# Performance work log

Hardware: AMD Instinct MI355X
Metric: run time of the kernel (lower is better)

The kernel has to match this reference:

```python
import jax, jax.numpy as jnp
import numpy as np

B, T, H = 4096, 1024, 15


def setup_inputs() -> dict:
    key = jax.random.key(0)
    ks = jax.random.split(key, 7)
    return {
        "x": jax.random.normal(ks[0], (B, T, 1), dtype=jnp.float32),
        "w_ih": jax.random.normal(ks[1], (H, 1), dtype=jnp.float32) * (1.0 / np.sqrt(H)),
        "w_hh": jax.random.normal(ks[2], (H, H), dtype=jnp.float32) * (1.0 / np.sqrt(H)),
        "b_ih": jax.random.normal(ks[3], (H,), dtype=jnp.float32) * (1.0 / np.sqrt(H)),
        "b_hh": jax.random.normal(ks[4], (H,), dtype=jnp.float32) * (1.0 / np.sqrt(H)),
        "w_lin": jax.random.normal(ks[5], (1, H), dtype=jnp.float32) * (1.0 / np.sqrt(H)),
        "b_lin": jax.random.normal(ks[6], (1,), dtype=jnp.float32) * (1.0 / np.sqrt(H)),
    }


def reference(x, w_ih, w_hh, b_ih, b_hh, w_lin, b_lin):
    # Single-layer tanh RNN (batch_first), then per-timestep linear head.
    # Precompute the input projection for all timesteps: [B, T, H]
    xp = jnp.einsum("bti,hi->bth", x, w_ih) + b_ih + b_hh
    xp_t = jnp.swapaxes(xp, 0, 1)  # [T, B, H] for scan over time

    def step(h, xt):
        # h: [B, H], xt: [B, H]
        h_new = jnp.tanh(xt + h @ w_hh.T)
        return h_new, h_new

    h0 = jnp.zeros((x.shape[0], w_hh.shape[0]), dtype=x.dtype)
    _, hs = jax.lax.scan(step, h0, xp_t)  # hs: [T, B, H]
    hs = jnp.swapaxes(hs, 0, 1)  # [B, T, H]
    return jnp.einsum("bth,oh->bto", hs, w_lin) + b_lin  # [B, T, 1]
```

## Files before the change

kernel.cpp:

```cpp
#include <hip/hip_runtime.h>

#define B_ 4096
#define T_ 1024
#define H_ 15

#define STEP(XT, ODST)                                                        \
  do {                                                                        \
    float bs_, cB_, cC_, cD_, e_;                                             \
    asm("v_fma_f32 %[bs], %[xt], %[wih], %[bias]\n\t"                         \
        "v_mul_f32_dpp %[acc], %[u], %[w1] row_ror:1 row_mask:0xf bank_mask:0xf\n\t"  \
        "v_mul_f32_dpp %[cB], %[u], %[w2] row_ror:2 row_mask:0xf bank_mask:0xf\n\t"   \
        "v_mul_f32_dpp %[cC], %[u], %[w3] row_ror:3 row_mask:0xf bank_mask:0xf\n\t"   \
        "v_fma_f32 %[cD], %[u], %[w0], %[bs]\n\t"                             \
        "v_fmac_f32_dpp %[acc], %[u], %[w5] row_ror:5 row_mask:0xf bank_mask:0xf\n\t" \
        "v_fmac_f32_dpp %[cB], %[u], %[w6] row_ror:6 row_mask:0xf bank_mask:0xf\n\t"  \
        "v_fmac_f32_dpp %[cC], %[u], %[w7] row_ror:7 row_mask:0xf bank_mask:0xf\n\t"  \
        "v_fmac_f32_dpp %[cD], %[u], %[w4] row_ror:4 row_mask:0xf bank_mask:0xf\n\t"  \
        "v_fmac_f32_dpp %[acc], %[u], %[w9] row_ror:9 row_mask:0xf bank_mask:0xf\n\t" \
        "v_fmac_f32_dpp %[cB], %[u], %[w10] row_ror:10 row_mask:0xf bank_mask:0xf\n\t" \
        "v_fmac_f32_dpp %[cC], %[u], %[w11] row_ror:11 row_mask:0xf bank_mask:0xf\n\t" \
        "v_fmac_f32_dpp %[cD], %[u], %[w8] row_ror:8 row_mask:0xf bank_mask:0xf\n\t"  \
        "v_fmac_f32_dpp %[acc], %[u], %[w13] row_ror:13 row_mask:0xf bank_mask:0xf\n\t" \
        "v_fmac_f32_dpp %[cB], %[u], %[w14] row_ror:14 row_mask:0xf bank_mask:0xf\n\t" \
        "v_fmac_f32_dpp %[cC], %[u], %[w15] row_ror:15 row_mask:0xf bank_mask:0xf\n\t" \
        "v_fmac_f32_dpp %[cD], %[u], %[w12] row_ror:12 row_mask:0xf bank_mask:0xf\n\t" \
        "v_add_f32 %[acc], %[acc], %[cB]\n\t"                                 \
        "v_add_f32 %[cC], %[cC], %[cD]\n\t"                                   \
        "v_add_f32 %[acc], %[acc], %[cC]\n\t"                                 \
        "v_exp_f32 %[e], %[acc]\n\t"                                          \
        "s_nop 0\n\t"                                                         \
        "v_add_f32 %[e], 1.0, %[e]\n\t"                                       \
        "v_rcp_f32 %[u], %[e]\n\t"                                            \
        "s_nop 0\n\t"                                                         \
        : [u] "+v"(u), [acc] "=&v"(ODST), [bs] "=&v"(bs_), [cB] "=&v"(cB_),   \
          [cC] "=&v"(cC_), [cD] "=&v"(cD_), [e] "=&v"(e_)                     \
        : [xt] "v"(XT), [wih] "v"(wih2), [bias] "v"(bias2),                   \
          [w0] "v"(wr[0]), [w1] "v"(wr[1]), [w2] "v"(wr[2]),                  \
          [w3] "v"(wr[3]), [w4] "v"(wr[4]), [w5] "v"(wr[5]),                  \
          [w6] "v"(wr[6]), [w7] "v"(wr[7]), [w8] "v"(wr[8]),                  \
          [w9] "v"(wr[9]), [w10] "v"(wr[10]), [w11] "v"(wr[11]),              \
          [w12] "v"(wr[12]), [w13] "v"(wr[13]), [w14] "v"(wr[14]),            \
          [w15] "v"(wr[15]));                                                 \
  } while (0)

#define POS(K, XV)                                                            \
  do {                                                                        \
    float o_;                                                                 \
    STEP(XV, o_);                                                             \
    osta[((K) + 3) & 3] = o_;                                                 \
    if (((K) & 3) == 0) {                                                     \
      if ((K) > 0 || t > 0) {                                                 \
        if (m == 15)                                                          \
          *(float4*)(ob + t + (K) - 4) =                                      \
              make_float4(osta[0], osta[1], osta[2], osta[3]);                \
      }                                                                       \
    }                                                                         \
    if (((K) & 3) == 3) {                                                     \
      int _tn = t + 32 + (((K) >> 2) << 2);                                   \
      if (_tn >= T_) _tn = 0;          \
      qq[(K) >> 2] = *(const float4*)(xb + _tn);                              \
    }                                                                         \
  } while (0)

__global__ __attribute__((amdgpu_flat_work_group_size(256, 256),
                          amdgpu_waves_per_eu(1, 1)))
void rnn_tanh_kernel(
    const float* __restrict__ x, const float* __restrict__ w_ih,
    const float* __restrict__ w_hh, const float* __restrict__ b_ih,
    const float* __restrict__ b_hh, const float* __restrict__ w_lin,
    const float* __restrict__ b_lin, float* __restrict__ out) {
  const int tid = threadIdx.x;
  const int m = tid & 15;
  const int b = blockIdx.x * 16 + (tid >> 4);

  const float S = 2.8853900817779268f;

  float wsum = b_lin[0];
  for (int j = 0; j < H_; ++j) wsum += w_lin[j];
  const float C = wsum;

  float wr[16];
#pragma unroll
  for (int n = 0; n < 16; ++n) {
    const int c = (m - n) & 15;
    if (m < H_)
      wr[n] = (c < H_) ? -2.0f * S * w_hh[m * H_ + c] : 0.0f;
    else
      wr[n] = (c < H_) ? -2.0f * w_lin[c] : 0.0f;
  }
  float rowsum = 0.0f;
  if (m < H_)
    for (int j = 0; j < H_; ++j) rowsum += w_hh[m * H_ + j];
  const float wih2  = (m < H_) ? S * w_ih[m] : 0.0f;
  const float bias2 = (m < H_) ? S * (b_ih[m] + b_hh[m] + rowsum) : C;

  const float* xb = x + (size_t)b * T_;
  float* ob = out + (size_t)b * T_;

  float u = 0.5f;
  asm("s_nop 1" : "+v"(u));
  float osta[4];

  float4 qq[8];
#pragma unroll
  for (int j = 0; j < 8; ++j) qq[j] = *(const float4*)(xb + 4 * j);

  for (int t = 0; t < T_; t += 32) {
    POS(0,  qq[0].x); POS(1,  qq[0].y); POS(2,  qq[0].z); POS(3,  qq[0].w);
    POS(4,  qq[1].x); POS(5,  qq[1].y); POS(6,  qq[1].z); POS(7,  qq[1].w);
    POS(8,  qq[2].x); POS(9,  qq[2].y); POS(10, qq[2].z); POS(11, qq[2].w);
    POS(12, qq[3].x); POS(13, qq[3].y); POS(14, qq[3].z); POS(15, qq[3].w);
    POS(16, qq[4].x); POS(17, qq[4].y); POS(18, qq[4].z); POS(19, qq[4].w);
    POS(20, qq[5].x); POS(21, qq[5].y); POS(22, qq[5].z); POS(23, qq[5].w);
    POS(24, qq[6].x); POS(25, qq[6].y); POS(26, qq[6].z); POS(27, qq[6].w);
    POS(28, qq[7].x); POS(29, qq[7].y); POS(30, qq[7].z); POS(31, qq[7].w);
  }

  {
    float o_;
    STEP(0.0f, o_);
    osta[3] = o_;
    if (m == 15)
      *(float4*)(ob + T_ - 4) = make_float4(osta[0], osta[1], osta[2], osta[3]);
  }
}

extern "C" void kernel_launch(void* const* d_in, const int* in_sizes, int n_in,
                              void* d_out, int out_size, void* d_ws, size_t ws_size,
                              hipStream_t stream) {
  (void)in_sizes; (void)n_in; (void)out_size; (void)d_ws; (void)ws_size;
  rnn_tanh_kernel<<<B_ / 16, 256, 0, stream>>>(
      (const float*)d_in[0], (const float*)d_in[1], (const float*)d_in[2],
      (const float*)d_in[3], (const float*)d_in[4], (const float*)d_in[5],
      (const float*)d_in[6], (float*)d_out);
}
```

Before: 141.7 us.

## Split each RNN row's dot product across two lane halves with permlane16 swap

Each batch row now uses 32 lanes instead of 16. Each 16-lane half computes 8 of the 16 rotated recurrent products, and the two partial sums are combined with v_permlane16_swap plus a DPP row_ror:8 move. This halves the serial FMA chain per timestep and doubles the grid, with waves_per_eu raised to 2. The cost is extra cross-lane latency from the swap, the nops and the DPP move, and twice as many lanes per batch row.

After: 167.4 us. 1.18x slower.

```diff
diff --git a/kernel.cpp b/kernel.cpp
--- a/kernel.cpp
+++ b/kernel.cpp
@@ -6,41 +6,36 @@
 
 #define STEP(XT, ODST)                                                        \
   do {                                                                        \
-    float bs_, cB_, cC_, cD_, e_;                                             \
+    float bs_, cA_, cB_, cC_, cD_, e_;                                        \
     asm("v_fma_f32 %[bs], %[xt], %[wih], %[bias]\n\t"                         \
-        "v_mul_f32_dpp %[acc], %[u], %[w1] row_ror:1 row_mask:0xf bank_mask:0xf\n\t"  \
-        "v_mul_f32_dpp %[cB], %[u], %[w2] row_ror:2 row_mask:0xf bank_mask:0xf\n\t"   \
-        "v_mul_f32_dpp %[cC], %[u], %[w3] row_ror:3 row_mask:0xf bank_mask:0xf\n\t"   \
-        "v_fma_f32 %[cD], %[u], %[w0], %[bs]\n\t"                             \
-        "v_fmac_f32_dpp %[acc], %[u], %[w5] row_ror:5 row_mask:0xf bank_mask:0xf\n\t" \
-        "v_fmac_f32_dpp %[cB], %[u], %[w6] row_ror:6 row_mask:0xf bank_mask:0xf\n\t"  \
-        "v_fmac_f32_dpp %[cC], %[u], %[w7] row_ror:7 row_mask:0xf bank_mask:0xf\n\t"  \
-        "v_fmac_f32_dpp %[cD], %[u], %[w4] row_ror:4 row_mask:0xf bank_mask:0xf\n\t"  \
-        "v_fmac_f32_dpp %[acc], %[u], %[w9] row_ror:9 row_mask:0xf bank_mask:0xf\n\t" \
-        "v_fmac_f32_dpp %[cB], %[u], %[w10] row_ror:10 row_mask:0xf bank_mask:0xf\n\t" \
-        "v_fmac_f32_dpp %[cC], %[u], %[w11] row_ror:11 row_mask:0xf bank_mask:0xf\n\t" \
-        "v_fmac_f32_dpp %[cD], %[u], %[w8] row_ror:8 row_mask:0xf bank_mask:0xf\n\t"  \
-        "v_fmac_f32_dpp %[acc], %[u], %[w13] row_ror:13 row_mask:0xf bank_mask:0xf\n\t" \
-        "v_fmac_f32_dpp %[cB], %[u], %[w14] row_ror:14 row_mask:0xf bank_mask:0xf\n\t" \
-        "v_fmac_f32_dpp %[cC], %[u], %[w15] row_ror:15 row_mask:0xf bank_mask:0xf\n\t" \
-        "v_fmac_f32_dpp %[cD], %[u], %[w12] row_ror:12 row_mask:0xf bank_mask:0xf\n\t" \
-        "v_add_f32 %[acc], %[acc], %[cB]\n\t"                                 \
+        "v_fma_f32 %[cA], %[u], %[w0], %[bs]\n\t"                             \
+        "v_mul_f32_dpp %[cB], %[u], %[w1] row_ror:1 row_mask:0xf bank_mask:0xf\n\t" \
+        "v_mul_f32_dpp %[cC], %[u], %[w2] row_ror:2 row_mask:0xf bank_mask:0xf\n\t" \
+        "v_mul_f32_dpp %[cD], %[u], %[w3] row_ror:3 row_mask:0xf bank_mask:0xf\n\t" \
+        "v_fmac_f32_dpp %[cA], %[u], %[w4] row_ror:4 row_mask:0xf bank_mask:0xf\n\t" \
+        "v_fmac_f32_dpp %[cB], %[u], %[w5] row_ror:5 row_mask:0xf bank_mask:0xf\n\t" \
+        "v_fmac_f32_dpp %[cC], %[u], %[w6] row_ror:6 row_mask:0xf bank_mask:0xf\n\t" \
+        "v_fmac_f32_dpp %[cD], %[u], %[w7] row_ror:7 row_mask:0xf bank_mask:0xf\n\t" \
+        "v_add_f32 %[cA], %[cA], %[cB]\n\t"                                   \
         "v_add_f32 %[cC], %[cC], %[cD]\n\t"                                   \
-        "v_add_f32 %[acc], %[acc], %[cC]\n\t"                                 \
-        "v_exp_f32 %[e], %[acc]\n\t"                                          \
+        "v_add_f32 %[cA], %[cA], %[cC]\n\t"                                   \
+        "v_mov_b32 %[cB], %[cA]\n\t"                                          \
+        "s_nop 1\n\t"                                                         \
+        "v_permlane16_swap_b32 %[cB], %[cA]\n\t"                              \
+        "v_add_f32 %[a], %[cB], %[cA]\n\t"                                    \
+        "s_nop 1\n\t"                                                         \
+        "v_mov_b32_dpp %[a], %[a] row_ror:8 row_mask:0xa bank_mask:0xf\n\t"   \
+        "v_exp_f32 %[e], %[a]\n\t"                                            \
         "s_nop 0\n\t"                                                         \
         "v_add_f32 %[e], 1.0, %[e]\n\t"                                       \
         "v_rcp_f32 %[u], %[e]\n\t"                                            \
         "s_nop 0\n\t"                                                         \
-        : [u] "+v"(u), [acc] "=&v"(ODST), [bs] "=&v"(bs_), [cB] "=&v"(cB_),   \
-          [cC] "=&v"(cC_), [cD] "=&v"(cD_), [e] "=&v"(e_)                     \
+        : [u] "+v"(u), [a] "=&v"(ODST), [bs] "=&v"(bs_), [cA] "=&v"(cA_),     \
+          [cB] "=&v"(cB_), [cC] "=&v"(cC_), [cD] "=&v"(cD_), [e] "=&v"(e_)    \
         : [xt] "v"(XT), [wih] "v"(wih2), [bias] "v"(bias2),                   \
           [w0] "v"(wr[0]), [w1] "v"(wr[1]), [w2] "v"(wr[2]),                  \
           [w3] "v"(wr[3]), [w4] "v"(wr[4]), [w5] "v"(wr[5]),                  \
-          [w6] "v"(wr[6]), [w7] "v"(wr[7]), [w8] "v"(wr[8]),                  \
-          [w9] "v"(wr[9]), [w10] "v"(wr[10]), [w11] "v"(wr[11]),              \
-          [w12] "v"(wr[12]), [w13] "v"(wr[13]), [w14] "v"(wr[14]),            \
-          [w15] "v"(wr[15]));                                                 \
+          [w6] "v"(wr[6]), [w7] "v"(wr[7]));                                  \
   } while (0)
 
 #define POS(K, XV)                                                            \
@@ -50,7 +45,7 @@
     osta[((K) + 3) & 3] = o_;                                                 \
     if (((K) & 3) == 0) {                                                     \
       if ((K) > 0 || t > 0) {                                                 \
-        if (m == 15)                                                          \
+        if (mm == 15)                                                         \
           *(float4*)(ob + t + (K) - 4) =                                      \
               make_float4(osta[0], osta[1], osta[2], osta[3]);                \
       }                                                                       \
@@ -63,7 +58,7 @@
   } while (0)
 
 __global__ __attribute__((amdgpu_flat_work_group_size(256, 256),
-                          amdgpu_waves_per_eu(1, 1)))
+                          amdgpu_waves_per_eu(2, 2)))
 void rnn_tanh_kernel(
     const float* __restrict__ x, const float* __restrict__ w_ih,
     const float* __restrict__ w_hh, const float* __restrict__ b_ih,
@@ -71,7 +66,9 @@
     const float* __restrict__ b_lin, float* __restrict__ out) {
   const int tid = threadIdx.x;
   const int m = tid & 15;
-  const int b = blockIdx.x * 16 + (tid >> 4);
+  const int h = (tid >> 4) & 1;
+  const int mm = tid & 31;
+  const int b = blockIdx.x * 8 + (tid >> 5);
 
   const float S = 2.8853900817779268f;
 
@@ -79,10 +76,10 @@
   for (int j = 0; j < H_; ++j) wsum += w_lin[j];
   const float C = wsum;
 
-  float wr[16];
+  float wr[8];
 #pragma unroll
-  for (int n = 0; n < 16; ++n) {
-    const int c = (m - n) & 15;
+  for (int n = 0; n < 8; ++n) {
+    const int c = (m + 8 * h - n) & 15;
     if (m < H_)
       wr[n] = (c < H_) ? -2.0f * S * w_hh[m * H_ + c] : 0.0f;
     else
@@ -91,8 +88,9 @@
   float rowsum = 0.0f;
   if (m < H_)
     for (int j = 0; j < H_; ++j) rowsum += w_hh[m * H_ + j];
-  const float wih2  = (m < H_) ? S * w_ih[m] : 0.0f;
-  const float bias2 = (m < H_) ? S * (b_ih[m] + b_hh[m] + rowsum) : C;
+  const float wih2  = (h == 0 && m < H_) ? S * w_ih[m] : 0.0f;
+  const float bias2 = (h == 0) ? ((m < H_) ? S * (b_ih[m] + b_hh[m] + rowsum) : C)
+                               : 0.0f;
 
   const float* xb = x + (size_t)b * T_;
   float* ob = out + (size_t)b * T_;
@@ -120,7 +118,7 @@
     float o_;
     STEP(0.0f, o_);
     osta[3] = o_;
-    if (m == 15)
+    if (mm == 15)
       *(float4*)(ob + T_ - 4) = make_float4(osta[0], osta[1], osta[2], osta[3]);
   }
 }
@@ -129,7 +127,7 @@
                               void* d_out, int out_size, void* d_ws, size_t ws_size,
                               hipStream_t stream) {
   (void)in_sizes; (void)n_in; (void)out_size; (void)d_ws; (void)ws_size;
-  rnn_tanh_kernel<<<B_ / 16, 256, 0, stream>>>(
+  rnn_tanh_kernel<<<B_ / 8, 256, 0, stream>>>(
       (const float*)d_in[0], (const float*)d_in[1], (const float*)d_in[2],
       (const float*)d_in[3], (const float*)d_in[4], (const float*)d_in[5],
       (const float*)d_in[6], (float*)d_out);
```
